# Kernel tuning notes

Measured on AMD Instinct MI355X. Metric: run time of the kernel, lower is better.

Reference implementation:

```python
import jax, jax.numpy as jnp
import numpy as np

MS_KS = 9
C = 256
BN_EPS = 1e-5


def setup_inputs() -> dict:
    key = jax.random.key(0)
    k1, k2, k3 = jax.random.split(key, 3)
    p2_r = jax.random.normal(k1, (2, C, 64, 128), dtype=jnp.float32)
    conv_w = jax.random.normal(k2, (C, C, 1, MS_KS), dtype=jnp.float32) * 0.02
    conv1_w = jax.random.normal(k3, (1, C, 1, 1), dtype=jnp.float32) * 0.05
    bn_gamma = jnp.ones((1,), jnp.float32)
    bn_beta = jnp.zeros((1,), jnp.float32)
    return dict(p2_r=p2_r, conv_w=conv_w, conv1_w=conv1_w,
                bn_gamma=bn_gamma, bn_beta=bn_beta)


def _scnn_pass(x, M):
    # x: [b,c,h,w]. Each step applies conv(1,ms_ks) to a width-1 column with
    # zero padding ms_ks//2 -> only the center tap contributes, i.e. a 256x256
    # channel matmul per column, followed by relu and residual add.
    cols = jnp.moveaxis(x, 3, 0)  # [w,b,c,h]
    def step(carry, col):
        new = col + jax.nn.relu(jnp.einsum('oc,bch->boh', M, carry))
        return new, new
    _, outs = jax.lax.scan(step, cols[0], cols[1:])
    outs = jnp.concatenate([cols[:1], outs], axis=0)[::-1]  # mirrors out[::-1]
    return jnp.moveaxis(outs, 0, 3)


def _upsample_bilinear_ac(x, factor=4):
    # F.interpolate(mode='bilinear', align_corners=True)
    b, c, h, w = x.shape
    Ho, Wo = factor * h, factor * w
    ys = jnp.arange(Ho, dtype=x.dtype) * ((h - 1) / (Ho - 1))
    xs = jnp.arange(Wo, dtype=x.dtype) * ((w - 1) / (Wo - 1))
    y0 = jnp.floor(ys).astype(jnp.int32)
    y1 = jnp.minimum(y0 + 1, h - 1)
    wy = (ys - y0.astype(x.dtype))[None, None, :, None]
    rows = x[:, :, y0, :] * (1 - wy) + x[:, :, y1, :] * wy  # [b,c,Ho,w]
    x0 = jnp.floor(xs).astype(jnp.int32)
    x1 = jnp.minimum(x0 + 1, w - 1)
    wx = (xs - x0.astype(x.dtype))[None, None, None, :]
    return rows[:, :, :, x0] * (1 - wx) + rows[:, :, :, x1] * wx


def reference(p2_r, conv_w, conv1_w, bn_gamma, bn_beta):
    M = conv_w[:, :, 0, MS_KS // 2]  # center tap, [c_out, c_in]
    x = _scnn_pass(p2_r, M)                     # reverse=False
    x = _scnn_pass(x[:, :, :, ::-1], M)         # reverse=True (slices[::-1])
    x = _upsample_bilinear_ac(x, 4)             # [b,256,4h,4w]
    x = jnp.einsum('oc,bchw->bohw', conv1_w[:, :, 0, 0], x)  # 1x1 conv -> 1 ch
    # BatchNorm2d(1), training-mode batch statistics (biased variance)
    mean = jnp.mean(x, axis=(0, 2, 3), keepdims=True)
    var = jnp.mean((x - mean) ** 2, axis=(0, 2, 3), keepdims=True)
    x = (x - mean) * jax.lax.rsqrt(var + BN_EPS)
    x = x * bn_gamma[None, :, None, None] + bn_beta[None, :, None, None]
    return jax.nn.sigmoid(x)
```

## Files before the change

kernel.cpp:

```cpp
#include <hip/hip_runtime.h>


typedef _Float16 f16x8 __attribute__((ext_vector_type(8)));
typedef _Float16 f16x4 __attribute__((ext_vector_type(4)));
typedef float    f32x4 __attribute__((ext_vector_type(4)));

extern "C" __global__ void k_extract(const float* __restrict__ convw,
                                     _Float16* __restrict__ Md) {
  int q = blockIdx.x * 256 + threadIdx.x;
  float4 v = ((const float4*)convw)[q];
  float vv[4] = {v.x, v.y, v.z, v.w};
  int f = q * 4;
#pragma unroll
  for (int e = 0; e < 4; ++e) {
    int flat = f + e;
    if (flat % 9 == 4) Md[flat / 9] = (_Float16)vv[e];
  }
}

struct SM {
  _Float16 cy[2][256];
  _Float16 pad_[32];
  _Float16 cz[2][256];
  float    sp[128 * 32];
};

extern "C" __global__ void __launch_bounds__(512, 2)
k_scan(const float* __restrict__ p2, const _Float16* __restrict__ Md,
       const float* __restrict__ conv1, float* __restrict__ sout,
       float* __restrict__ stats) {
  __shared__ SM sm;
  const int tid  = threadIdx.x;
  const int l    = tid & 63;
  const int r    = tid >> 6;
  const int col  = l & 15;
  const int quad = l >> 4;
  const int b    = blockIdx.x >> 6;
  const int h    = blockIdx.x & 63;

  if (blockIdx.x == 0 && tid == 0) { stats[0] = 0.f; stats[1] = 0.f; }

  const bool isY = (col == 0);
  const bool isZ = (col == 1);

  const int m0 = (r * 2 + 0) * 16 + quad * 4;
  const int m1 = (r * 2 + 1) * 16 + quad * 4;

  f16x8 A0[8], A1[8];
#pragma unroll
  for (int ch = 0; ch < 8; ++ch) {
    A0[ch] = *(const f16x8*)(Md + ((r*2+0)*16 + col) * 256 + ch*32 + quad*8);
    A1[ch] = *(const f16x8*)(Md + ((r*2+1)*16 + col) * 256 + ch*32 + quad*8);
  }

  const float* pbase = p2 + (size_t)b * 2097152 + (size_t)h * 128;

  float vva[4], vvb[4];
  {
    float c0a[4], c0b[4];
    if (isY || isZ) {
#pragma unroll
      for (int i = 0; i < 4; ++i) {
        c0a[i] = pbase[(size_t)(m0 + i) * 8192];
        c0b[i] = pbase[(size_t)(m1 + i) * 8192];
      }
    }
    if (isY) {
      f16x4 pa, pb;
#pragma unroll
      for (int i = 0; i < 4; ++i) { pa[i] = (_Float16)c0a[i]; pb[i] = (_Float16)c0b[i]; }
      *(f16x4*)(sm.cy[0] + m0) = pa; *(f16x4*)(sm.cy[0] + m1) = pb;
      *(f16x4*)(sm.cz[0] + m0) = pa; *(f16x4*)(sm.cz[0] + m1) = pb;
    }
    if (isZ) {
#pragma unroll
      for (int i = 0; i < 4; ++i) { vva[i] = conv1[m0 + i]; vvb[i] = conv1[m1 + i]; }
      float p = 0.f;
#pragma unroll
      for (int i = 0; i < 4; ++i) p += vva[i] * c0a[i] + vvb[i] * c0b[i];
      sm.sp[0 * 32 + r * 4 + quad] = p;
    }
  }

  float cca[4], ccb[4], cna[4], cnb[4];
  if (isY) {
#pragma unroll
    for (int i = 0; i < 4; ++i) {
      cca[i] = pbase[(size_t)(m0 + i) * 8192 + 1];
      ccb[i] = pbase[(size_t)(m1 + i) * 8192 + 1];
      cna[i] = pbase[(size_t)(m0 + i) * 8192 + 2];
      cnb[i] = pbase[(size_t)(m1 + i) * 8192 + 2];
    }
  }
  __syncthreads();

  const _Float16* selA = ((l & 1) ? sm.cz[0] : sm.cy[0]) + quad * 8;
  const _Float16* selB = ((l & 1) ? sm.cz[1] : sm.cy[1]) + quad * 8;

#define STEP(W, SELP, WY, WZ, CA, CB)                                          \
  do {                                                                         \
    f16x8 B[8];                                                                \
    _Pragma("unroll")                                                          \
    for (int ch = 0; ch < 8; ++ch)                                             \
      B[ch] = *(const f16x8*)((SELP) + ch * 32);                               \
    f32x4 a00 = {0.f,0.f,0.f,0.f}, a01 = {0.f,0.f,0.f,0.f};                    \
    f32x4 a10 = {0.f,0.f,0.f,0.f}, a11 = {0.f,0.f,0.f,0.f};                    \
    _Pragma("unroll")                                                          \
    for (int ch = 0; ch < 4; ++ch) {                                           \
      a00 = __builtin_amdgcn_mfma_f32_16x16x32_f16(A0[ch],   B[ch],   a00,0,0,0);\
      a10 = __builtin_amdgcn_mfma_f32_16x16x32_f16(A1[ch],   B[ch],   a10,0,0,0);\
      a01 = __builtin_amdgcn_mfma_f32_16x16x32_f16(A0[ch+4], B[ch+4], a01,0,0,0);\
      a11 = __builtin_amdgcn_mfma_f32_16x16x32_f16(A1[ch+4], B[ch+4], a11,0,0,0);\
    }                                                                          \
    f32x4 acc0 = a00 + a01, acc1 = a10 + a11;                                  \
    f16x4 yh0 = {}, yh1 = {};                                                  \
    if (isY) {                                                                 \
      _Pragma("unroll")                                                        \
      for (int i = 0; i < 4; ++i) {                                            \
        yh0[i] = (_Float16)((CA)[i] + fmaxf(acc0[i], 0.f));                    \
        yh1[i] = (_Float16)((CB)[i] + fmaxf(acc1[i], 0.f));                    \
      }                                                                        \
      *(f16x4*)((WY) + m0) = yh0;                                              \
      *(f16x4*)((WY) + m1) = yh1;                                              \
      if ((W) + 2 < 128) {                                                     \
        _Pragma("unroll")                                                      \
        for (int i = 0; i < 4; ++i) {                                          \
          (CA)[i] = pbase[(size_t)(m0 + i) * 8192 + (W) + 2];                  \
          (CB)[i] = pbase[(size_t)(m1 + i) * 8192 + (W) + 2];                  \
        }                                                                      \
      }                                                                        \
    }                                                                          \
    int2 u0 = __builtin_bit_cast(int2, yh0), u1 = __builtin_bit_cast(int2, yh1);\
    u0.x = __shfl(u0.x, l & 62, 64); u0.y = __shfl(u0.y, l & 62, 64);          \
    u1.x = __shfl(u1.x, l & 62, 64); u1.y = __shfl(u1.y, l & 62, 64);          \
    f16x4 ys0 = __builtin_bit_cast(f16x4, u0), ys1 = __builtin_bit_cast(f16x4, u1);\
    if (isZ) {                                                                 \
      f16x4 zh0, zh1;                                                          \
      float p = 0.f;                                                           \
      _Pragma("unroll")                                                        \
      for (int i = 0; i < 4; ++i) {                                            \
        float z0 = (float)ys0[i] + fmaxf(acc0[i], 0.f);                        \
        float z1 = (float)ys1[i] + fmaxf(acc1[i], 0.f);                        \
        zh0[i] = (_Float16)z0; zh1[i] = (_Float16)z1;                          \
        p += vva[i] * z0 + vvb[i] * z1;                                        \
      }                                                                        \
      *(f16x4*)((WZ) + m0) = zh0;                                              \
      *(f16x4*)((WZ) + m1) = zh1;                                              \
      sm.sp[(W) * 32 + r * 4 + quad] = p;                                      \
    }                                                                          \
    __syncthreads();                                                           \
  } while (0)

#pragma unroll 1
  for (int w = 1; w < 127; w += 2) {
    STEP(w,     selA, sm.cy[1], sm.cz[1], cca, ccb);
    STEP(w + 1, selB, sm.cy[0], sm.cz[0], cna, cnb);
  }
  STEP(127, selA, sm.cy[1], sm.cz[1], cca, ccb);
#undef STEP

  if (tid < 128) {
    const float4* q = (const float4*)(sm.sp + tid * 32);
    float s = 0.f;
#pragma unroll
    for (int j = 0; j < 8; ++j) { float4 t4 = q[j]; s += t4.x + t4.y + t4.z + t4.w; }
    sout[(blockIdx.x << 7) + (127 - tid)] = s;
  }
}

static __device__ __forceinline__ float bilin(const float* __restrict__ s,
                                              int idx) {
  int bb  = idx >> 17;
  int rem = idx & 131071;
  int ho  = rem >> 9;
  int wo  = rem & 511;
  const float SY = 63.0f / 255.0f, SX = 127.0f / 511.0f;
  float fy = (float)ho * SY;
  int y0 = (int)fy; int y1 = min(y0 + 1, 63); float wy = fy - (float)y0;
  float fx = (float)wo * SX;
  int x0 = (int)fx; int x1 = min(x0 + 1, 127); float wx = fx - (float)x0;
  const float* sb = s + bb * 8192;
  float cA = sb[y0 * 128 + x0] * (1.f - wy) + sb[y1 * 128 + x0] * wy;
  float cB = sb[y0 * 128 + x1] * (1.f - wy) + sb[y1 * 128 + x1] * wy;
  return cA * (1.f - wx) + cB * wx;
}

extern "C" __global__ void k_stats(const float* __restrict__ s,
                                   float* __restrict__ stats) {
  int tid  = threadIdx.x;
  int base = blockIdx.x * 1024 + tid;
  float sum = 0.f, ssq = 0.f;
#pragma unroll
  for (int i = 0; i < 4; ++i) {
    float u = bilin(s, base + i * 256);
    sum += u; ssq += u * u;
  }
#pragma unroll
  for (int off = 32; off > 0; off >>= 1) {
    sum += __shfl_xor(sum, off, 64);
    ssq += __shfl_xor(ssq, off, 64);
  }
  __shared__ float ls[4], lq[4];
  int wv = tid >> 6;
  if ((tid & 63) == 0) { ls[wv] = sum; lq[wv] = ssq; }
  __syncthreads();
  if (tid == 0) {
    atomicAdd(&stats[0], ls[0] + ls[1] + ls[2] + ls[3]);
    atomicAdd(&stats[1], lq[0] + lq[1] + lq[2] + lq[3]);
  }
}

extern "C" __global__ void k_norm(const float* __restrict__ s,
                                  const float* __restrict__ stats,
                                  const float* __restrict__ gamma,
                                  const float* __restrict__ beta,
                                  float* __restrict__ out) {
  int tid  = threadIdx.x;
  int base = blockIdx.x * 1024 + tid;
  const float invN = 1.f / 262144.f;
  float mean  = stats[0] * invN;
  float var   = stats[1] * invN - mean * mean;
  float scale = rsqrtf(var + 1e-5f) * gamma[0];
  float bias  = beta[0] - mean * scale;
#pragma unroll
  for (int i = 0; i < 4; ++i) {
    int idx = base + i * 256;
    float u = bilin(s, idx);
    float x = u * scale + bias;
    out[idx] = 1.f / (1.f + __expf(-x));
  }
}

extern "C" void kernel_launch(void* const* d_in, const int* in_sizes, int n_in,
                              void* d_out, int out_size, void* d_ws, size_t ws_size,
                              hipStream_t stream) {
  const float* p2    = (const float*)d_in[0];
  const float* convw = (const float*)d_in[1];
  const float* conv1 = (const float*)d_in[2];
  const float* gamma = (const float*)d_in[3];
  const float* beta  = (const float*)d_in[4];
  float* out = (float*)d_out;

  char* ws = (char*)d_ws;
  float*    s     = (float*)ws;
  float*    stats = (float*)(ws + 65536);
  _Float16* Md    = (_Float16*)(ws + 65792);

  hipLaunchKernelGGL(k_extract, dim3(576), dim3(256), 0, stream, convw, Md);
  hipLaunchKernelGGL(k_scan,    dim3(128), dim3(512), 0, stream, p2, Md, conv1, s, stats);
  hipLaunchKernelGGL(k_stats,   dim3(256), dim3(256), 0, stream, s, stats);
  hipLaunchKernelGGL(k_norm,    dim3(256), dim3(256), 0, stream, s, stats, gamma, beta, out);
}
```

Before: 184.8 us.

## Fuse weight extraction into scan, stage columns via LDS, merge stats and norm kernels

Removes the separate weight-extraction kernel by having each scan block gather the center-tap weights directly from conv_w into registers. Column inputs are now prefetched in 16-wide tiles into a double-buffered LDS area with global_load_lds, replacing the per-step scalar global loads. The stats and normalize kernels are merged into one, using an atomic counter as a grid-wide barrier so the bilinear values are computed once. The grid barrier needs all 256 blocks to be resident at once, and the strided weight gather is less coalesced.

```diff
diff --git a/kernel.cpp b/kernel.cpp
--- a/kernel.cpp
+++ b/kernel.cpp
@@ -5,17 +5,10 @@
 typedef _Float16 f16x4 __attribute__((ext_vector_type(4)));
 typedef float    f32x4 __attribute__((ext_vector_type(4)));
 
-extern "C" __global__ void k_extract(const float* __restrict__ convw,
-                                     _Float16* __restrict__ Md) {
-  int q = blockIdx.x * 256 + threadIdx.x;
-  float4 v = ((const float4*)convw)[q];
-  float vv[4] = {v.x, v.y, v.z, v.w};
-  int f = q * 4;
-#pragma unroll
-  for (int e = 0; e < 4; ++e) {
-    int flat = f + e;
-    if (flat % 9 == 4) Md[flat / 9] = (_Float16)vv[e];
-  }
+static __device__ __forceinline__ void load_lds16(const float* g, void* lds) {
+  __builtin_amdgcn_global_load_lds(
+      (const __attribute__((address_space(1))) void*)g,
+      (__attribute__((address_space(3))) void*)lds, 16, 0, 0);
 }
 
 struct SM {
@@ -23,12 +16,13 @@
   _Float16 pad_[32];
   _Float16 cz[2][256];
   float    sp[128 * 32];
+  float    cbuf[2][256][16];
 };
 
 extern "C" __global__ void __launch_bounds__(512, 2)
-k_scan(const float* __restrict__ p2, const _Float16* __restrict__ Md,
+k_scan(const float* __restrict__ p2, const float* __restrict__ convw,
        const float* __restrict__ conv1, float* __restrict__ sout,
-       float* __restrict__ stats) {
+       float* __restrict__ stats, unsigned int* __restrict__ cnt) {
   __shared__ SM sm;
   const int tid  = threadIdx.x;
   const int l    = tid & 63;
@@ -38,22 +32,35 @@
   const int b    = blockIdx.x >> 6;
   const int h    = blockIdx.x & 63;
 
-  if (blockIdx.x == 0 && tid == 0) { stats[0] = 0.f; stats[1] = 0.f; }
+  if (blockIdx.x == 0 && tid == 0) { stats[0] = 0.f; stats[1] = 0.f; *cnt = 0u; }
 
   const bool isY = (col == 0);
   const bool isZ = (col == 1);
 
-  const int m0 = (r * 2 + 0) * 16 + quad * 4;
-  const int m1 = (r * 2 + 1) * 16 + quad * 4;
-
+  const int m0 = r * 32 + quad * 4;
+  const int m1 = m0 + 16;
+
+  const float* pbase = p2 + (size_t)b * 2097152 + (size_t)h * 128;
+
+#pragma unroll
+  for (int j = 0; j < 2; ++j) {
+    const float* g = pbase + (size_t)(r * 32 + j * 16 + (l >> 2)) * 8192 + (l & 3) * 4;
+    load_lds16(g, &sm.cbuf[0][r * 32 + j * 16][0]);
+  }
+
+  const int row0 = r * 32 + col;
+  const int row1 = row0 + 16;
+  const int koff = quad * 8;
   f16x8 A0[8], A1[8];
 #pragma unroll
   for (int ch = 0; ch < 8; ++ch) {
-    A0[ch] = *(const f16x8*)(Md + ((r*2+0)*16 + col) * 256 + ch*32 + quad*8);
-    A1[ch] = *(const f16x8*)(Md + ((r*2+1)*16 + col) * 256 + ch*32 + quad*8);
-  }
-
-  const float* pbase = p2 + (size_t)b * 2097152 + (size_t)h * 128;
+#pragma unroll
+    for (int j = 0; j < 8; ++j) {
+      int k = ch * 32 + koff + j;
+      A0[ch][j] = (_Float16)convw[(size_t)row0 * 2304 + k * 9 + 4];
+      A1[ch][j] = (_Float16)convw[(size_t)row1 * 2304 + k * 9 + 4];
+    }
+  }
 
   float vva[4], vvb[4];
   {
@@ -81,24 +88,23 @@
       sm.sp[0 * 32 + r * 4 + quad] = p;
     }
   }
-
-  float cca[4], ccb[4], cna[4], cnb[4];
-  if (isY) {
-#pragma unroll
-    for (int i = 0; i < 4; ++i) {
-      cca[i] = pbase[(size_t)(m0 + i) * 8192 + 1];
-      ccb[i] = pbase[(size_t)(m1 + i) * 8192 + 1];
-      cna[i] = pbase[(size_t)(m0 + i) * 8192 + 2];
-      cnb[i] = pbase[(size_t)(m1 + i) * 8192 + 2];
-    }
-  }
   __syncthreads();
 
   const _Float16* selA = ((l & 1) ? sm.cz[0] : sm.cy[0]) + quad * 8;
   const _Float16* selB = ((l & 1) ? sm.cz[1] : sm.cy[1]) + quad * 8;
 
-#define STEP(W, SELP, WY, WZ, CA, CB)                                          \
+#define STEP(W, SELP, WY, WZ, DOSTAGE)                                         \
   do {                                                                         \
+    if (DOSTAGE && ((W) & 15) == 1 && (W) < 113) {                             \
+      int t1 = ((W) >> 4) + 1;                             \
+      int bs = t1 & 1;                                                         \
+      _Pragma("unroll")                                                        \
+      for (int j = 0; j < 2; ++j) {                                            \
+        const float* g = pbase + (size_t)(r * 32 + j * 16 + (l >> 2)) * 8192   \
+                         + t1 * 16 + (l & 3) * 4;                              \
+        load_lds16(g, &sm.cbuf[bs][r * 32 + j * 16][0]);                       \
+      }                                                                        \
+    }                                                                          \
     f16x8 B[8];                                                                \
     _Pragma("unroll")                                                          \
     for (int ch = 0; ch < 8; ++ch)                                             \
@@ -113,22 +119,16 @@
       a11 = __builtin_amdgcn_mfma_f32_16x16x32_f16(A1[ch+4], B[ch+4], a11,0,0,0);\
     }                                                                          \
     f32x4 acc0 = a00 + a01, acc1 = a10 + a11;                                  \
+    const float* cptr = &sm.cbuf[((W) >> 4) & 1][0][(W) & 15];                 \
     f16x4 yh0 = {}, yh1 = {};                                                  \
     if (isY) {                                                                 \
       _Pragma("unroll")                                                        \
       for (int i = 0; i < 4; ++i) {                                            \
-        yh0[i] = (_Float16)((CA)[i] + fmaxf(acc0[i], 0.f));                    \
-        yh1[i] = (_Float16)((CB)[i] + fmaxf(acc1[i], 0.f));                    \
+        yh0[i] = (_Float16)(cptr[(m0 + i) * 16] + fmaxf(acc0[i], 0.f));        \
+        yh1[i] = (_Float16)(cptr[(m1 + i) * 16] + fmaxf(acc1[i], 0.f));        \
       }                                                                        \
       *(f16x4*)((WY) + m0) = yh0;                                              \
       *(f16x4*)((WY) + m1) = yh1;                                              \
-      if ((W) + 2 < 128) {                                                     \
-        _Pragma("unroll")                                                      \
-        for (int i = 0; i < 4; ++i) {                                          \
-          (CA)[i] = pbase[(size_t)(m0 + i) * 8192 + (W) + 2];                  \
-          (CB)[i] = pbase[(size_t)(m1 + i) * 8192 + (W) + 2];                  \
-        }                                                                      \
-      }                                                                        \
     }                                                                          \
     int2 u0 = __builtin_bit_cast(int2, yh0), u1 = __builtin_bit_cast(int2, yh1);\
     u0.x = __shfl(u0.x, l & 62, 64); u0.y = __shfl(u0.y, l & 62, 64);          \
@@ -153,10 +153,10 @@
 
 #pragma unroll 1
   for (int w = 1; w < 127; w += 2) {
-    STEP(w,     selA, sm.cy[1], sm.cz[1], cca, ccb);
-    STEP(w + 1, selB, sm.cy[0], sm.cz[0], cna, cnb);
-  }
-  STEP(127, selA, sm.cy[1], sm.cz[1], cca, ccb);
+    STEP(w,     selA, sm.cy[1], sm.cz[1], 1);
+    STEP(w + 1, selB, sm.cy[0], sm.cz[0], 0);
+  }
+  STEP(127, selA, sm.cy[1], sm.cz[1], 0);
 #undef STEP
 
   if (tid < 128) {
@@ -185,15 +185,18 @@
   return cA * (1.f - wx) + cB * wx;
 }
 
-extern "C" __global__ void k_stats(const float* __restrict__ s,
-                                   float* __restrict__ stats) {
+extern "C" __global__ void __launch_bounds__(256, 1)
+k_statsnorm(const float* __restrict__ s, float* __restrict__ stats,
+            unsigned int* __restrict__ cnt, const float* __restrict__ gamma,
+            const float* __restrict__ beta, float* __restrict__ out) {
   int tid  = threadIdx.x;
   int base = blockIdx.x * 1024 + tid;
+  float u[4];
   float sum = 0.f, ssq = 0.f;
 #pragma unroll
   for (int i = 0; i < 4; ++i) {
-    float u = bilin(s, base + i * 256);
-    sum += u; ssq += u * u;
+    u[i] = bilin(s, base + i * 256);
+    sum += u[i]; ssq += u[i] * u[i];
   }
 #pragma unroll
   for (int off = 32; off > 0; off >>= 1) {
@@ -205,29 +208,26 @@
   if ((tid & 63) == 0) { ls[wv] = sum; lq[wv] = ssq; }
   __syncthreads();
   if (tid == 0) {
-    atomicAdd(&stats[0], ls[0] + ls[1] + ls[2] + ls[3]);
-    atomicAdd(&stats[1], lq[0] + lq[1] + lq[2] + lq[3]);
-  }
-}
-
-extern "C" __global__ void k_norm(const float* __restrict__ s,
-                                  const float* __restrict__ stats,
-                                  const float* __restrict__ gamma,
-                                  const float* __restrict__ beta,
-                                  float* __restrict__ out) {
-  int tid  = threadIdx.x;
-  int base = blockIdx.x * 1024 + tid;
+    float bsum = ls[0] + ls[1] + ls[2] + ls[3];
+    float bssq = lq[0] + lq[1] + lq[2] + lq[3];
+    __hip_atomic_fetch_add(&stats[0], bsum, __ATOMIC_RELAXED, __HIP_MEMORY_SCOPE_AGENT);
+    __hip_atomic_fetch_add(&stats[1], bssq, __ATOMIC_RELAXED, __HIP_MEMORY_SCOPE_AGENT);
+    __hip_atomic_fetch_add(cnt, 1u, __ATOMIC_RELEASE, __HIP_MEMORY_SCOPE_AGENT);
+    while (__hip_atomic_load(cnt, __ATOMIC_ACQUIRE, __HIP_MEMORY_SCOPE_AGENT) < 256u)
+      __builtin_amdgcn_s_sleep(8);
+  }
+  __syncthreads();
+  float s0 = __hip_atomic_load(&stats[0], __ATOMIC_RELAXED, __HIP_MEMORY_SCOPE_AGENT);
+  float s1 = __hip_atomic_load(&stats[1], __ATOMIC_RELAXED, __HIP_MEMORY_SCOPE_AGENT);
   const float invN = 1.f / 262144.f;
-  float mean  = stats[0] * invN;
-  float var   = stats[1] * invN - mean * mean;
+  float mean  = s0 * invN;
+  float var   = s1 * invN - mean * mean;
   float scale = rsqrtf(var + 1e-5f) * gamma[0];
   float bias  = beta[0] - mean * scale;
 #pragma unroll
   for (int i = 0; i < 4; ++i) {
-    int idx = base + i * 256;
-    float u = bilin(s, idx);
-    float x = u * scale + bias;
-    out[idx] = 1.f / (1.f + __expf(-x));
+    float x = u[i] * scale + bias;
+    out[base + i * 256] = 1.f / (1.f + __expf(-x));
   }
 }
 
@@ -242,12 +242,12 @@
   float* out = (float*)d_out;
 
   char* ws = (char*)d_ws;
-  float*    s     = (float*)ws;
-  float*    stats = (float*)(ws + 65536);
-  _Float16* Md    = (_Float16*)(ws + 65792);
-
-  hipLaunchKernelGGL(k_extract, dim3(576), dim3(256), 0, stream, convw, Md);
-  hipLaunchKernelGGL(k_scan,    dim3(128), dim3(512), 0, stream, p2, Md, conv1, s, stats);
-  hipLaunchKernelGGL(k_stats,   dim3(256), dim3(256), 0, stream, s, stats);
-  hipLaunchKernelGGL(k_norm,    dim3(256), dim3(256), 0, stream, s, stats, gamma, beta, out);
-}
+  float*        s     = (float*)ws;
+  float*        stats = (float*)(ws + 65536);
+  unsigned int* cnt   = (unsigned int*)(ws + 65544);
+
+  hipLaunchKernelGGL(k_scan,      dim3(128), dim3(512), 0, stream,
+                     p2, convw, conv1, s, stats, cnt);
+  hipLaunchKernelGGL(k_statsnorm, dim3(256), dim3(256), 0, stream,
+                     s, stats, cnt, gamma, beta, out);
+}
```

Measured after the change: 222.8 us. +20.6%, slower.
